# Performance work log

Measured on AMD Instinct MI355X. Metric: run time of the kernel, lower is better.

The kernel has to match this reference:

```python
import jax, jax.numpy as jnp
import numpy as np

N_BITS = 8
QMAX = float(2 ** (N_BITS - 1) - 1)  # 127 for 8-bit symmetric
EPS = 1e-8


def fake_quant(x, axes):
    """Symmetric fake quantization (quantize + dequantize) over `axes`.

    scale = amax(|x|) / qmax over the reduction axes, then
    round/clamp to the integer grid and rescale back to float.
    """
    amax = jnp.max(jnp.abs(x), axis=axes, keepdims=True)
    scale = jnp.maximum(amax, EPS) / QMAX
    q = jnp.clip(jnp.round(x / scale), -QMAX, QMAX)
    return q * scale


def setup_inputs() -> dict:
    key = jax.random.key(0)
    k1, k2, k3 = jax.random.split(key, 3)
    B, S, D_IN, D_OUT = 4, 2048, 4096, 4096
    inp = {
        "input": jax.random.normal(k1, (B, S, D_IN), dtype=jnp.float32),
        "weight": jax.random.normal(k2, (D_OUT, D_IN), dtype=jnp.float32) * (1.0 / np.sqrt(D_IN)),
        "bias": jax.random.normal(k3, (D_OUT,), dtype=jnp.float32),
    }
    return inp


def reference(input, weight, bias):
    # act quantizer: per-example scale over dims (-2, -1) i.e. (seq, hidden)
    x_q = fake_quant(input, axes=(-2, -1))
    # weight quantizer: per-tensor scale
    w_q = fake_quant(weight, axes=(0, 1))
    # F.linear: input @ weight.T + bias
    return jnp.einsum("bsi,oi->bso", x_q, w_q) + bias
```

## Files before the change

### kernel.cpp

```cpp
#include <hip/hip_runtime.h>

typedef __attribute__((ext_vector_type(4))) int i32x4;

#define AS1 __attribute__((address_space(1)))
#define AS3 __attribute__((address_space(3)))

static constexpr int  S_LEN = 2048, DIN = 4096, DOUT = 4096, NBATCH = 4;
static constexpr long XTOT = (long)NBATCH * S_LEN * DIN;
static constexpr long WTOT = (long)DOUT * DIN;
static constexpr float QMAXF = 127.0f;
static constexpr float EPSF  = 1e-8f;

__global__ void amax_k(const float* __restrict__ x, const float* __restrict__ w,
                       float* __restrict__ amax) {
  int y = blockIdx.y;
  const float4* src;
  long n4;
  if (y < NBATCH) { src = (const float4*)(x + (long)y * S_LEN * DIN); n4 = (long)S_LEN * DIN / 4; }
  else            { src = (const float4*)w; n4 = WTOT / 4; }
  float m = 0.f;
  for (long i = (long)blockIdx.x * blockDim.x + threadIdx.x; i < n4;
       i += (long)gridDim.x * blockDim.x) {
    float4 v = src[i];
    m = fmaxf(m, fmaxf(fmaxf(fabsf(v.x), fabsf(v.y)), fmaxf(fabsf(v.z), fabsf(v.w))));
  }
  for (int off = 32; off; off >>= 1) m = fmaxf(m, __shfl_xor(m, off, 64));
  __shared__ float sm[4];
  if ((threadIdx.x & 63) == 0) sm[threadIdx.x >> 6] = m;
  __syncthreads();
  if (threadIdx.x == 0) {
    m = fmaxf(fmaxf(sm[0], sm[1]), fmaxf(sm[2], sm[3]));
    atomicMax((unsigned int*)&amax[y], __float_as_uint(m));
  }
}

__global__ void quant_k(const float* __restrict__ x, const float* __restrict__ w,
                        const float* __restrict__ amax,
                        char* __restrict__ qx, char* __restrict__ qw) {
  long idx = ((long)blockIdx.x * blockDim.x + threadIdx.x) * 16;
  const float* src;
  char* dst;
  float scale;
  if (idx < XTOT) {
    int b = (int)(idx >> 23);
    scale = fmaxf(amax[b], EPSF) / QMAXF;
    src = x + idx;
    dst = qx + idx;
  } else {
    long j = idx - XTOT;
    scale = fmaxf(amax[4], EPSF) / QMAXF;
    src = w + j;
    dst = qw + j;
  }
  int words[4];
#pragma unroll
  for (int g = 0; g < 4; ++g) {
    float4 v = ((const float4*)src)[g];
    float r0 = fminf(fmaxf(rintf(v.x / scale), -QMAXF), QMAXF);
    float r1 = fminf(fmaxf(rintf(v.y / scale), -QMAXF), QMAXF);
    float r2 = fminf(fmaxf(rintf(v.z / scale), -QMAXF), QMAXF);
    float r3 = fminf(fmaxf(rintf(v.w / scale), -QMAXF), QMAXF);
    words[g] = ((int)r0 & 255) | (((int)r1 & 255) << 8) |
               (((int)r2 & 255) << 16) | ((int)r3 << 24);
  }
  *(i32x4*)dst = *(const i32x4*)words;
}

__global__ __launch_bounds__(256) void gemm_k(
    const char* __restrict__ qx, const char* __restrict__ qw,
    const float* __restrict__ amax, const float* __restrict__ bias,
    float* __restrict__ out) {
  constexpr int BM = 128, BN = 128, BK = 64, K = 4096, N = 4096;
  __shared__ __align__(16) char As[BM * BK];
  __shared__ __align__(16) char Bs[BN * BK];

  int cpx = gridDim.x >> 3;
  int sw  = (blockIdx.x & 7) * cpx + (blockIdx.x >> 3);
  int tm = sw >> 5;
  int tn = sw & 31;
  long brow = (long)tm * BM;
  long bcol = (long)tn * BN;

  int tid = threadIdx.x;
  int lane = tid & 63, wid = tid >> 6;
  int wr = wid >> 1, wc = wid & 1;

  int r0 = tid >> 2;
  int p  = tid & 3;
  int lu = p ^ ((r0 >> 1) & 3);
  const char* gA0 = qx + (brow + r0) * (long)K + lu * 16;
  const char* gA1 = gA0 + 64 * (long)K;
  const char* gB0 = qw + (bcol + r0) * (long)K + lu * 16;
  const char* gB1 = gB0 + 64 * (long)K;

  int offA[4], offB[4];
#pragma unroll
  for (int f = 0; f < 4; ++f) {
    int rowa = wr * 64 + f * 16 + (lane & 15);
    offA[f] = rowa * 64 + (((lane >> 4) ^ ((rowa >> 1) & 3)) * 16);
    int rowb = wc * 64 + f * 16 + (lane & 15);
    offB[f] = rowb * 64 + (((lane >> 4) ^ ((rowb >> 1) & 3)) * 16);
  }

  i32x4 acc[4][4];
#pragma unroll
  for (int i = 0; i < 4; ++i)
#pragma unroll
    for (int j = 0; j < 4; ++j) acc[i][j] = 0;

  for (int kt = 0; kt < K / BK; ++kt) {
    long ko = (long)kt * BK;
    __builtin_amdgcn_global_load_lds((const AS1 void*)(gA0 + ko),
                                     (AS3 void*)(As + wid * 1024), 16, 0, 0);
    __builtin_amdgcn_global_load_lds((const AS1 void*)(gA1 + ko),
                                     (AS3 void*)(As + 4096 + wid * 1024), 16, 0, 0);
    __builtin_amdgcn_global_load_lds((const AS1 void*)(gB0 + ko),
                                     (AS3 void*)(Bs + wid * 1024), 16, 0, 0);
    __builtin_amdgcn_global_load_lds((const AS1 void*)(gB1 + ko),
                                     (AS3 void*)(Bs + 4096 + wid * 1024), 16, 0, 0);
    asm volatile("s_waitcnt vmcnt(0)" ::: "memory");
    __syncthreads();

    i32x4 a[4], b[4];
#pragma unroll
    for (int f = 0; f < 4; ++f) a[f] = *(const i32x4*)(As + offA[f]);
#pragma unroll
    for (int f = 0; f < 4; ++f) b[f] = *(const i32x4*)(Bs + offB[f]);
#pragma unroll
    for (int m = 0; m < 4; ++m)
#pragma unroll
      for (int n = 0; n < 4; ++n)
        acc[m][n] = __builtin_amdgcn_mfma_i32_16x16x64_i8(a[m], b[n], acc[m][n], 0, 0, 0);

    __syncthreads();
  }

  float ax = amax[(int)(brow >> 11)];
  float aw = amax[4];
  float scale = (fmaxf(ax, EPSF) / QMAXF) * (fmaxf(aw, EPSF) / QMAXF);
#pragma unroll
  for (int fn = 0; fn < 4; ++fn) {
    int col = (int)bcol + wc * 64 + fn * 16 + (lane & 15);
    float bv = bias[col];
#pragma unroll
    for (int fm = 0; fm < 4; ++fm) {
      long rbase = brow + wr * 64 + fm * 16 + ((lane >> 4) * 4);
#pragma unroll
      for (int r = 0; r < 4; ++r) {
        out[(rbase + r) * N + col] = scale * (float)acc[fm][fn][r] + bv;
      }
    }
  }
}

extern "C" void kernel_launch(void* const* d_in, const int* in_sizes, int n_in,
                              void* d_out, int out_size, void* d_ws, size_t ws_size,
                              hipStream_t stream) {
  const float* x    = (const float*)d_in[0];
  const float* w    = (const float*)d_in[1];
  const float* bias = (const float*)d_in[2];
  float* out = (float*)d_out;

  float* amax = (float*)d_ws;
  char* qx = (char*)d_ws + 256;
  char* qw = qx + XTOT;
  if (ws_size < (size_t)(256 + XTOT + WTOT)) return;

  hipMemsetAsync(d_ws, 0, 32, stream);

  amax_k<<<dim3(256, 5), 256, 0, stream>>>(x, w, amax);

  long total = XTOT + WTOT;
  int qblocks = (int)(total / 16 / 256);
  quant_k<<<qblocks, 256, 0, stream>>>(x, w, amax, qx, qw);

  gemm_k<<<(8192 / 128) * (4096 / 128), 256, 0, stream>>>(qx, qw, amax, bias, out);
}
```

Baseline: 465.9 us.

## Rewrite int8 GEMM as 256x256 double-buffered pipelined kernel and flatten amax grid

The GEMM moves to 256x256 tiles with 8 waves, BK=128 and a double-buffered 128KB LDS. Global-to-LDS loads for the next tiles are interleaved with quarter-tile MFMA phases, using barriers and s_setprio to overlap memory with compute. This removes the single-buffer load/wait/compute serialization of the old kernel and raises data reuse per tile. The amax kernel is also reshaped into a flat grid with a fixed unrolled 16-iteration loop per thread. The costs are higher register pressure from the 8x4 accumulator and only 512 blocks, which may limit occupancy.

```diff
diff --git a/kernel.cpp b/kernel.cpp
--- a/kernel.cpp
+++ b/kernel.cpp
@@ -11,18 +11,30 @@
 static constexpr float QMAXF = 127.0f;
 static constexpr float EPSF  = 1e-8f;
 
-__global__ void amax_k(const float* __restrict__ x, const float* __restrict__ w,
-                       float* __restrict__ amax) {
-  int y = blockIdx.y;
-  const float4* src;
-  long n4;
-  if (y < NBATCH) { src = (const float4*)(x + (long)y * S_LEN * DIN); n4 = (long)S_LEN * DIN / 4; }
-  else            { src = (const float4*)w; n4 = WTOT / 4; }
+__global__ __launch_bounds__(256) void amax_k(const float* __restrict__ x,
+                                              const float* __restrict__ w,
+                                              float* __restrict__ amax) {
+  int bid = blockIdx.x;
   float m = 0.f;
-  for (long i = (long)blockIdx.x * blockDim.x + threadIdx.x; i < n4;
-       i += (long)gridDim.x * blockDim.x) {
-    float4 v = src[i];
-    m = fmaxf(m, fmaxf(fmaxf(fabsf(v.x), fabsf(v.y)), fmaxf(fabsf(v.z), fabsf(v.w))));
+  int slot;
+  if (bid < 2048) {
+    slot = bid >> 9;
+    const float4* s = (const float4*)(x + ((long)slot << 23));
+    long i = ((long)(bid & 511) << 8) + threadIdx.x;
+#pragma unroll
+    for (int it = 0; it < 16; ++it) {
+      float4 v = s[i + (long)it * (512 * 256)];
+      m = fmaxf(m, fmaxf(fmaxf(fabsf(v.x), fabsf(v.y)), fmaxf(fabsf(v.z), fabsf(v.w))));
+    }
+  } else {
+    slot = 4;
+    const float4* s = (const float4*)w;
+    long i = ((long)(bid - 2048) << 8) + threadIdx.x;
+#pragma unroll
+    for (int it = 0; it < 16; ++it) {
+      float4 v = s[i + (long)it * (1024 * 256)];
+      m = fmaxf(m, fmaxf(fmaxf(fabsf(v.x), fabsf(v.y)), fmaxf(fabsf(v.z), fabsf(v.w))));
+    }
   }
   for (int off = 32; off; off >>= 1) m = fmaxf(m, __shfl_xor(m, off, 64));
   __shared__ float sm[4];
@@ -30,13 +42,14 @@
   __syncthreads();
   if (threadIdx.x == 0) {
     m = fmaxf(fmaxf(sm[0], sm[1]), fmaxf(sm[2], sm[3]));
-    atomicMax((unsigned int*)&amax[y], __float_as_uint(m));
-  }
-}
-
-__global__ void quant_k(const float* __restrict__ x, const float* __restrict__ w,
-                        const float* __restrict__ amax,
-                        char* __restrict__ qx, char* __restrict__ qw) {
+    atomicMax((unsigned int*)&amax[slot], __float_as_uint(m));
+  }
+}
+
+__global__ __launch_bounds__(256) void quant_k(const float* __restrict__ x,
+                                               const float* __restrict__ w,
+                                               const float* __restrict__ amax,
+                                               char* __restrict__ qx, char* __restrict__ qw) {
   long idx = ((long)blockIdx.x * blockDim.x + threadIdx.x) * 16;
   const float* src;
   char* dst;
@@ -66,89 +79,141 @@
   *(i32x4*)dst = *(const i32x4*)words;
 }
 
-__global__ __launch_bounds__(256) void gemm_k(
+__device__ __forceinline__ void load_half_a(i32x4 a[4][2], const char* p, int u0, int u1) {
+#pragma unroll
+  for (int f = 0; f < 4; ++f) {
+    a[f][0] = *(const i32x4*)(p + f * 2048 + u0);
+    a[f][1] = *(const i32x4*)(p + f * 2048 + u1);
+  }
+}
+__device__ __forceinline__ void load_half_b(i32x4 b[2][2], const char* p, int u0, int u1) {
+#pragma unroll
+  for (int g = 0; g < 2; ++g) {
+    b[g][0] = *(const i32x4*)(p + g * 2048 + u0);
+    b[g][1] = *(const i32x4*)(p + g * 2048 + u1);
+  }
+}
+template <int QA, int QB>
+__device__ __forceinline__ void do_mfma(i32x4 acc[8][4], const i32x4 a[4][2],
+                                        const i32x4 b[2][2]) {
+#pragma unroll
+  for (int f = 0; f < 4; ++f)
+#pragma unroll
+    for (int g = 0; g < 2; ++g) {
+      i32x4 c = acc[QA * 4 + f][QB * 2 + g];
+      c = __builtin_amdgcn_mfma_i32_16x16x64_i8(a[f][0], b[g][0], c, 0, 0, 0);
+      c = __builtin_amdgcn_mfma_i32_16x16x64_i8(a[f][1], b[g][1], c, 0, 0, 0);
+      acc[QA * 4 + f][QB * 2 + g] = c;
+    }
+}
+__device__ __forceinline__ void stage2(const char* g0, long K, char* ld) {
+  __builtin_amdgcn_global_load_lds((const AS1 void*)g0, (AS3 void*)ld, 16, 0, 0);
+  __builtin_amdgcn_global_load_lds((const AS1 void*)(g0 + 64 * K), (AS3 void*)(ld + 8192), 16, 0, 0);
+}
+
+__global__ __launch_bounds__(512, 2) void gemm_k(
     const char* __restrict__ qx, const char* __restrict__ qw,
     const float* __restrict__ amax, const float* __restrict__ bias,
     float* __restrict__ out) {
-  constexpr int BM = 128, BN = 128, BK = 64, K = 4096, N = 4096;
-  __shared__ __align__(16) char As[BM * BK];
-  __shared__ __align__(16) char Bs[BN * BK];
-
-  int cpx = gridDim.x >> 3;
-  int sw  = (blockIdx.x & 7) * cpx + (blockIdx.x >> 3);
-  int tm = sw >> 5;
-  int tn = sw & 31;
-  long brow = (long)tm * BM;
-  long bcol = (long)tn * BN;
+  constexpr int K = 4096, N = 4096, NT = 32;
+  __shared__ __align__(16) char lds[131072];
+  char* ldsA = lds;
+  char* ldsB = lds + 65536;
+
+  int cpx = (int)gridDim.x >> 3;
+  int sw  = ((int)blockIdx.x & 7) * cpx + ((int)blockIdx.x >> 3);
+  int tm = sw >> 4, tn = sw & 15;
+  long brow = (long)tm * 256, bcol = (long)tn * 256;
 
   int tid = threadIdx.x;
-  int lane = tid & 63, wid = tid >> 6;
-  int wr = wid >> 1, wc = wid & 1;
-
-  int r0 = tid >> 2;
-  int p  = tid & 3;
-  int lu = p ^ ((r0 >> 1) & 3);
-  const char* gA0 = qx + (brow + r0) * (long)K + lu * 16;
-  const char* gA1 = gA0 + 64 * (long)K;
-  const char* gB0 = qw + (bcol + r0) * (long)K + lu * 16;
-  const char* gB1 = gB0 + 64 * (long)K;
-
-  int offA[4], offB[4];
-#pragma unroll
-  for (int f = 0; f < 4; ++f) {
-    int rowa = wr * 64 + f * 16 + (lane & 15);
-    offA[f] = rowa * 64 + (((lane >> 4) ^ ((rowa >> 1) & 3)) * 16);
-    int rowb = wc * 64 + f * 16 + (lane & 15);
-    offB[f] = rowb * 64 + (((lane >> 4) ^ ((rowb >> 1) & 3)) * 16);
-  }
-
-  i32x4 acc[4][4];
-#pragma unroll
-  for (int i = 0; i < 4; ++i)
+  int l = tid & 63, wid = tid >> 6;
+  int wr = wid >> 2, wc = wid & 3;
+
+  int sl = (l >> 1) & 7;
+  int u0 = (((l >> 4) ^ sl)) << 4;
+  int u1 = ((((l >> 4) | 4) ^ sl)) << 4;
+  int rA = (wr * 128 + (l & 15)) * 128;
+  int rB = (wc * 64 + (l & 15)) * 128;
+
+  int sr0 = tid >> 3;
+  int lu16 = ((tid & 7) ^ ((sr0 >> 1) & 7)) << 4;
+  const char* gA = qx + (brow + sr0) * (long)K + lu16;
+  const char* gB = qw + (bcol + sr0) * (long)K + lu16;
+
+  i32x4 acc[8][4];
+#pragma unroll
+  for (int i = 0; i < 8; ++i)
 #pragma unroll
     for (int j = 0; j < 4; ++j) acc[i][j] = 0;
-
-  for (int kt = 0; kt < K / BK; ++kt) {
-    long ko = (long)kt * BK;
-    __builtin_amdgcn_global_load_lds((const AS1 void*)(gA0 + ko),
-                                     (AS3 void*)(As + wid * 1024), 16, 0, 0);
-    __builtin_amdgcn_global_load_lds((const AS1 void*)(gA1 + ko),
-                                     (AS3 void*)(As + 4096 + wid * 1024), 16, 0, 0);
-    __builtin_amdgcn_global_load_lds((const AS1 void*)(gB0 + ko),
-                                     (AS3 void*)(Bs + wid * 1024), 16, 0, 0);
-    __builtin_amdgcn_global_load_lds((const AS1 void*)(gB1 + ko),
-                                     (AS3 void*)(Bs + 4096 + wid * 1024), 16, 0, 0);
-    asm volatile("s_waitcnt vmcnt(0)" ::: "memory");
-    __syncthreads();
-
-    i32x4 a[4], b[4];
-#pragma unroll
-    for (int f = 0; f < 4; ++f) a[f] = *(const i32x4*)(As + offA[f]);
-#pragma unroll
-    for (int f = 0; f < 4; ++f) b[f] = *(const i32x4*)(Bs + offB[f]);
-#pragma unroll
-    for (int m = 0; m < 4; ++m)
-#pragma unroll
-      for (int n = 0; n < 4; ++n)
-        acc[m][n] = __builtin_amdgcn_mfma_i32_16x16x64_i8(a[m], b[n], acc[m][n], 0, 0, 0);
-
-    __syncthreads();
+  i32x4 a[4][2], b0[2][2], b1[2][2];
+
+  stage2(gA, K, ldsA + tid * 16);
+  stage2(gB, K, ldsB + tid * 16);
+  stage2(gA + 128 * (long)K, K, ldsA + 16384 + tid * 16);
+  stage2(gB + 128 * (long)K, K, ldsB + 16384 + tid * 16);
+  stage2(gA + 128, K, ldsA + 32768 + tid * 16);
+  stage2(gB + 128, K, ldsB + 32768 + tid * 16);
+  asm volatile("s_waitcnt vmcnt(4)" ::: "memory");
+  __builtin_amdgcn_s_barrier();
+
+  for (int t = 0; t < NT; ++t) {
+    int d = t & 1;
+    const char* cA = ldsA + d * 32768;
+    const char* cB = ldsB + d * 32768;
+    load_half_a(a, cA + rA, u0, u1);
+    load_half_b(b0, cB + rB, u0, u1);
+    if (t + 1 < NT)
+      stage2(gA + 128 * (long)K + (t + 1) * 128, K,
+             ldsA + ((t + 1) & 1) * 32768 + 16384 + tid * 16);
+    __builtin_amdgcn_s_barrier();
+    asm volatile("s_waitcnt lgkmcnt(0)" ::: "memory");
+    __builtin_amdgcn_s_setprio(1);
+    do_mfma<0, 0>(acc, a, b0);
+    __builtin_amdgcn_s_setprio(0);
+    __builtin_amdgcn_s_barrier();
+    load_half_b(b1, cB + rB + 4096, u0, u1);
+    if (t + 1 < NT)
+      stage2(gB + 128 * (long)K + (t + 1) * 128, K,
+             ldsB + ((t + 1) & 1) * 32768 + 16384 + tid * 16);
+    __builtin_amdgcn_s_barrier();
+    asm volatile("s_waitcnt lgkmcnt(0)" ::: "memory");
+    __builtin_amdgcn_s_setprio(1);
+    do_mfma<0, 1>(acc, a, b1);
+    __builtin_amdgcn_s_setprio(0);
+    __builtin_amdgcn_s_barrier();
+    load_half_a(a, cA + rA + 8192, u0, u1);
+    __builtin_amdgcn_s_barrier();
+    asm volatile("s_waitcnt lgkmcnt(0)" ::: "memory");
+    __builtin_amdgcn_s_setprio(1);
+    do_mfma<1, 1>(acc, a, b1);
+    __builtin_amdgcn_s_setprio(0);
+    __builtin_amdgcn_s_barrier();
+    if (t + 2 < NT) {
+      stage2(gA + (t + 2) * 128, K, ldsA + d * 32768 + tid * 16);
+      stage2(gB + (t + 2) * 128, K, ldsB + d * 32768 + tid * 16);
+    }
+    __builtin_amdgcn_s_barrier();
+    __builtin_amdgcn_s_setprio(1);
+    do_mfma<1, 0>(acc, a, b0);
+    __builtin_amdgcn_s_setprio(0);
+    if (t < NT - 2) asm volatile("s_waitcnt vmcnt(4)" ::: "memory");
+    else            asm volatile("s_waitcnt vmcnt(0)" ::: "memory");
+    __builtin_amdgcn_s_barrier();
   }
 
   float ax = amax[(int)(brow >> 11)];
   float aw = amax[4];
   float scale = (fmaxf(ax, EPSF) / QMAXF) * (fmaxf(aw, EPSF) / QMAXF);
 #pragma unroll
-  for (int fn = 0; fn < 4; ++fn) {
-    int col = (int)bcol + wc * 64 + fn * 16 + (lane & 15);
+  for (int fb = 0; fb < 4; ++fb) {
+    int col = (int)bcol + wc * 64 + fb * 16 + (l & 15);
     float bv = bias[col];
 #pragma unroll
-    for (int fm = 0; fm < 4; ++fm) {
-      long rbase = brow + wr * 64 + fm * 16 + ((lane >> 4) * 4);
-#pragma unroll
-      for (int r = 0; r < 4; ++r) {
-        out[(rbase + r) * N + col] = scale * (float)acc[fm][fn][r] + bv;
-      }
+    for (int fa = 0; fa < 8; ++fa) {
+      long r0 = brow + wr * 128 + fa * 16 + ((l >> 4) * 4);
+#pragma unroll
+      for (int r = 0; r < 4; ++r)
+        out[(r0 + r) * N + col] = scale * (float)acc[fa][fb][r] + bv;
     }
   }
 }
@@ -168,11 +233,11 @@
 
   hipMemsetAsync(d_ws, 0, 32, stream);
 
-  amax_k<<<dim3(256, 5), 256, 0, stream>>>(x, w, amax);
+  amax_k<<<3072, 256, 0, stream>>>(x, w, amax);
 
   long total = XTOT + WTOT;
   int qblocks = (int)(total / 16 / 256);
   quant_k<<<qblocks, 256, 0, stream>>>(x, w, amax, qx, qw);
 
-  gemm_k<<<(8192 / 128) * (4096 / 128), 256, 0, stream>>>(qx, qw, amax, bias, out);
-}
+  gemm_k<<<512, 512, 0, stream>>>(qx, qw, amax, bias, out);
+}
```

Measured after the change: 429.0 us. 7.9% less time.
